# Kernel tuning notes

Hardware: AMD Instinct MI355X
Metric: run time of the kernel (lower is better)

Reference implementation:

```python
import math
import jax, jax.numpy as jnp
import numpy as np

D_MODEL = 1024
NUM_HEADS = 16
D_HEAD = D_MODEL // NUM_HEADS  # 64
K_S = 32  # sparse top-k keys kept per query
B, N = 2, 2048


def setup_inputs() -> dict:
    key = jax.random.key(0)
    ks = jax.random.split(key, 9)
    s = 1.0 / math.sqrt(D_MODEL)
    return {
        "x": jax.random.normal(ks[0], (B, N, D_MODEL), dtype=jnp.float32),
        "Wq": jax.random.normal(ks[1], (D_MODEL, D_MODEL), dtype=jnp.float32) * s,
        "bq": jnp.zeros((D_MODEL,), dtype=jnp.float32),
        "Wk": jax.random.normal(ks[2], (D_MODEL, D_MODEL), dtype=jnp.float32) * s,
        "bk": jnp.zeros((D_MODEL,), dtype=jnp.float32),
        "Wv": jax.random.normal(ks[3], (D_MODEL, D_MODEL), dtype=jnp.float32) * s,
        "bv": jnp.zeros((D_MODEL,), dtype=jnp.float32),
        "Wo": jax.random.normal(ks[4], (D_MODEL, D_MODEL), dtype=jnp.float32) * s,
        "bo": jnp.zeros((D_MODEL,), dtype=jnp.float32),
    }


def _attn(x, Wq, bq, Wk, bk, Wv, bv, Wo, bo):
    b, n, _ = x.shape
    # projections (torch Linear: y = x W^T + b)
    q = (x @ Wq.T + bq).reshape(b, n, NUM_HEADS, D_HEAD).transpose(0, 2, 1, 3)
    k = (x @ Wk.T + bk).reshape(b, n, NUM_HEADS, D_HEAD).transpose(0, 2, 1, 3)
    v = (x @ Wv.T + bv).reshape(b, n, NUM_HEADS, D_HEAD).transpose(0, 2, 1, 3)
    # full scores [b, H, n, n]
    scores = jnp.einsum("bhqd,bhkd->bhqk", q, k) / math.sqrt(D_HEAD)
    # causal mask (triu above diagonal -> -inf)
    causal = jnp.triu(jnp.ones((n, n), dtype=bool), k=1)
    neg_inf = jnp.array(-jnp.inf, dtype=scores.dtype)
    scores = jnp.where(causal, neg_inf, scores)
    # sparse top-k: keep only K_S largest scores per query row
    vals, idx = jax.lax.top_k(scores, K_S)
    masked = jnp.full_like(scores, -jnp.inf)
    masked = jnp.put_along_axis(masked, idx, vals, axis=-1, inplace=False)
    attn = jax.nn.softmax(masked, axis=-1)  # dropout p=0.0 -> identity
    out = jnp.einsum("bhqk,bhkd->bhqd", attn, v)
    out = out.transpose(0, 2, 1, 3).reshape(b, n, D_MODEL)
    y = out @ Wo.T + bo
    return y, attn.mean(axis=1)


def reference(x, Wq, bq, Wk, bk, Wv, bv, Wo, bo):
    return _attn(x, Wq, bq, Wk, bk, Wv, bv, Wo, bo)
```

## Files before the change

### kernel.cpp

```cpp
#include <hip/hip_runtime.h>
#include <hip/hip_bf16.h>
#include <math.h>

#define BATCH   2
#define NTOK    2048
#define DMODEL  1024
#define HEADS   16
#define DHEAD   64
#define KSEL    32
#define MROWS   (BATCH * NTOK)
#define NBLK8   (NTOK / 8)
#define TPW     8

typedef short     bf16x8 __attribute__((ext_vector_type(8)));
typedef float     f32x4  __attribute__((ext_vector_type(4)));
typedef unsigned short ushort_t;
typedef unsigned long long u64;

#define GLOAD_LDS16(g, l) \
    __builtin_amdgcn_global_load_lds((const __attribute__((address_space(1))) void*)(g), \
                                     (__attribute__((address_space(3))) void*)(l), 16, 0, 0)

__device__ __forceinline__ ushort_t f2bf(float f) {
    unsigned u = __float_as_uint(f);
    unsigned r = (u + 0x7FFFu + ((u >> 16) & 1u)) >> 16;
    return (ushort_t)r;
}
__device__ __forceinline__ float bf2f(ushort_t h) {
    return __uint_as_float(((unsigned)h) << 16);
}

__device__ __forceinline__ void conv_body(const float* __restrict__ in,
                                          ushort_t* __restrict__ hi,
                                          ushort_t* __restrict__ lo, int n, int i)
{
    if (i + 3 < n) {
        const float4 v = *(const float4*)(in + i);
        ushort4 ph, pl;
        ph.x = f2bf(v.x); pl.x = f2bf(v.x - bf2f(ph.x));
        ph.y = f2bf(v.y); pl.y = f2bf(v.y - bf2f(ph.y));
        ph.z = f2bf(v.z); pl.z = f2bf(v.z - bf2f(ph.z));
        ph.w = f2bf(v.w); pl.w = f2bf(v.w - bf2f(ph.w));
        *(ushort4*)(hi + i) = ph;
        *(ushort4*)(lo + i) = pl;
    }
}

__global__ __launch_bounds__(256) void conv_split(const float* __restrict__ in,
                                                  ushort_t* __restrict__ hi,
                                                  ushort_t* __restrict__ lo, int n)
{
    const int i = (blockIdx.x * 256 + threadIdx.x) * 4;
    conv_body(in, hi, lo, n, i);
}

__global__ __launch_bounds__(256) void conv_split4(const float* __restrict__ i0, ushort_t* __restrict__ h0, ushort_t* __restrict__ l0,
                                                   const float* __restrict__ i1, ushort_t* __restrict__ h1, ushort_t* __restrict__ l1,
                                                   const float* __restrict__ i2, ushort_t* __restrict__ h2, ushort_t* __restrict__ l2,
                                                   const float* __restrict__ i3, ushort_t* __restrict__ h3, ushort_t* __restrict__ l3,
                                                   int n)
{
    const int w = blockIdx.y;
    const float* in = (w == 0) ? i0 : (w == 1) ? i1 : (w == 2) ? i2 : i3;
    ushort_t* hi = (w == 0) ? h0 : (w == 1) ? h1 : (w == 2) ? h2 : h3;
    ushort_t* lo = (w == 0) ? l0 : (w == 1) ? l1 : (w == 2) ? l2 : l3;
    const int i = (blockIdx.x * 256 + threadIdx.x) * 4;
    conv_body(in, hi, lo, n, i);
}

__global__ __launch_bounds__(256) void zero_fill(float* __restrict__ p, int n4)
{
    const int i = blockIdx.x * 256 + threadIdx.x;
    if (i < n4) ((float4*)p)[i] = (float4){0.f, 0.f, 0.f, 0.f};
}

__device__ __forceinline__ unsigned mono_key(float f) {
    const unsigned u = __float_as_uint(f);
    return (u ^ (unsigned)(((int)u >> 31) | 0x80000000)) + 1u;
}
__device__ __forceinline__ float unmono(unsigned m) {
    const unsigned u = m - 1u;
    return __uint_as_float(u ^ (unsigned)(((int)(~u) >> 31) | 0x80000000));
}

__global__ __launch_bounds__(256, 3) void gemm_split_mfma(const ushort_t* __restrict__ Ahi,
                                                          const ushort_t* __restrict__ Alo,
                                                          const ushort_t* __restrict__ Bhi,
                                                          const ushort_t* __restrict__ Blo,
                                                          const float* __restrict__ bias,
                                                          float* __restrict__ out,
                                                          ushort_t* __restrict__ oh,
                                                          ushort_t* __restrict__ om,
                                                          ushort_t* __restrict__ ol,
                                                          int mode)
{
    __shared__ ushort_t smem[2 * 12288];

    const int tid  = threadIdx.x;
    const int wave = tid >> 6;
    const int lane = tid & 63;
    const int fr   = lane & 15;
    const int k8   = lane >> 4;
    const int m0 = blockIdx.x * 128;
    const int n0 = blockIdx.y * 64;

    f32x4 acc[2][4];
#pragma unroll
    for (int i = 0; i < 2; ++i)
#pragma unroll
        for (int j = 0; j < 4; ++j) acc[i][j] = (f32x4){0.f, 0.f, 0.f, 0.f};

#define STAGE(bufsel, k0v) do {                                                \
        ushort_t* dst_ = smem + (bufsel) * 12288;                              \
        _Pragma("unroll")                                                      \
        for (int i_ = 0; i_ < 2; ++i_) {                                       \
            const int c_ = i_ * 256 + tid;                                     \
            const int row_ = c_ >> 2;                                          \
            const int g_ = (c_ & 3) ^ ((row_ >> 1) & 3);                       \
            const size_t ga_ = (size_t)(m0 + row_) * DMODEL + (k0v) + g_ * 8;  \
            GLOAD_LDS16(Ahi + ga_, dst_ + (size_t)c_ * 8);                     \
            GLOAD_LDS16(Alo + ga_, dst_ + 4096 + (size_t)c_ * 8);              \
        }                                                                      \
        {                                                                      \
            const int c_ = tid;                                                \
            const int row_ = c_ >> 2;                                          \
            const int g_ = (c_ & 3) ^ ((row_ >> 1) & 3);                       \
            const size_t gb_ = (size_t)(n0 + row_) * DMODEL + (k0v) + g_ * 8;  \
            GLOAD_LDS16(Bhi + gb_, dst_ + 8192 + (size_t)c_ * 8);              \
            GLOAD_LDS16(Blo + gb_, dst_ + 10240 + (size_t)c_ * 8);             \
        }                                                                      \
    } while (0)

    STAGE(0, 0);
    int cur = 0;

    for (int k0 = 0; k0 < DMODEL; k0 += 32) {
        __syncthreads();
        if (k0 + 32 < DMODEL) STAGE(cur ^ 1, k0 + 32);

        const ushort_t* buf = smem + cur * 12288;
        bf16x8 afh[2], afl[2], bfh[4], bfl[4];
#pragma unroll
        for (int mi = 0; mi < 2; ++mi) {
            const int r = wave * 32 + mi * 16 + fr;
            const int ro = r * 32 + (k8 ^ ((r >> 1) & 3)) * 8;
            afh[mi] = *(const bf16x8*)(buf + ro);
            afl[mi] = *(const bf16x8*)(buf + 4096 + ro);
        }
#pragma unroll
        for (int ni = 0; ni < 4; ++ni) {
            const int r = ni * 16 + fr;
            const int ro = r * 32 + (k8 ^ ((r >> 1) & 3)) * 8;
            bfh[ni] = *(const bf16x8*)(buf + 8192 + ro);
            bfl[ni] = *(const bf16x8*)(buf + 10240 + ro);
        }

#pragma unroll
        for (int mi = 0; mi < 2; ++mi)
#pragma unroll
            for (int ni = 0; ni < 4; ++ni) {
                acc[mi][ni] = __builtin_amdgcn_mfma_f32_16x16x32_bf16(afh[mi], bfl[ni], acc[mi][ni], 0, 0, 0);
                acc[mi][ni] = __builtin_amdgcn_mfma_f32_16x16x32_bf16(afl[mi], bfh[ni], acc[mi][ni], 0, 0, 0);
                acc[mi][ni] = __builtin_amdgcn_mfma_f32_16x16x32_bf16(afh[mi], bfh[ni], acc[mi][ni], 0, 0, 0);
            }
        cur ^= 1;
    }
#undef STAGE

#pragma unroll
    for (int ni = 0; ni < 4; ++ni) {
        const int o = n0 + ni * 16 + (lane & 15);
        const float bv = bias[o];
#pragma unroll
        for (int mi = 0; mi < 2; ++mi) {
#pragma unroll
            for (int reg = 0; reg < 4; ++reg) {
                const int m = m0 + wave * 32 + mi * 16 + ((lane >> 4) << 2) + reg;
                const float v = acc[mi][ni][reg] + bv;
                if (mode == 0) {
                    out[(size_t)m * DMODEL + o] = v;
                } else {
                    const int bb = m >> 11;
                    const int n  = m & 2047;
                    const int hd = o >> 6;
                    const int d  = o & 63;
                    const size_t off = (((size_t)(bb * HEADS + hd)) * NTOK + n) * DHEAD + d;
                    if (mode == 1) {
                        out[off] = v;
                    } else {
                        const ushort_t h1 = f2bf(v);
                        const float r1 = v - bf2f(h1);
                        const ushort_t m1 = f2bf(r1);
                        const ushort_t l1 = f2bf(r1 - bf2f(m1));
                        oh[off] = h1; om[off] = m1; ol[off] = l1;
                    }
                }
            }
        }
    }
}

__global__ __launch_bounds__(256, 3) void score_mfma(const ushort_t* __restrict__ Qh,
                                                     const ushort_t* __restrict__ Qm,
                                                     const ushort_t* __restrict__ Ql,
                                                     const ushort_t* __restrict__ Kh,
                                                     const ushort_t* __restrict__ Km,
                                                     const ushort_t* __restrict__ Kl,
                                                     unsigned* __restrict__ S,
                                                     unsigned* __restrict__ Smax,
                                                     int q0, int QC)
{
    const int ks = blockIdx.x;
    const int qt = blockIdx.y;
    const int bh = blockIdx.z;
    const int qbase = q0 + qt * 128;
    const int ktmax = ((qbase + 127) >> 6) + 1;
    const int kt0 = ks * TPW;
    if (kt0 >= ktmax) return;
    const int kt1 = (kt0 + TPW < ktmax) ? (kt0 + TPW) : ktmax;

    __shared__ ushort_t smem[2 * 12288];

    const int tid  = threadIdx.x;
    const int wave = tid >> 6;
    const int lane = tid & 63;
    const int l15  = lane & 15;
    const int l4   = lane >> 4;

    const size_t qgbase = ((size_t)bh * NTOK + qbase) * DHEAD;

    bf16x8 qf[3][2][2];
#pragma unroll
    for (int p = 0; p < 3; ++p) {
        const ushort_t* Qp = (p == 0) ? Qh : (p == 1) ? Qm : Ql;
#pragma unroll
        for (int j = 0; j < 2; ++j) {
            const int r = wave * 32 + j * 16 + l15;
#pragma unroll
            for (int h = 0; h < 2; ++h)
                qf[p][j][h] = *(const bf16x8*)(Qp + qgbase + (size_t)r * DHEAD + (h * 4 + l4) * 8);
        }
    }

#define STAGE_K(bufsel, ktv) do {                                              \
        const size_t kg_ = ((size_t)bh * NTOK + (ktv) * 64) * DHEAD;           \
        _Pragma("unroll")                                                      \
        for (int i_ = 0; i_ < 2; ++i_) {                                       \
            const int c_ = i_ * 256 + tid;                                     \
            const int row_ = c_ >> 3;                                          \
            const int g_ = (c_ & 7) ^ (row_ & 7);                              \
            const size_t goff_ = kg_ + (size_t)row_ * DHEAD + g_ * 8;          \
            ushort_t* dst_ = smem + (bufsel) * 12288 + (size_t)c_ * 8;         \
            GLOAD_LDS16(Kh + goff_, dst_ + 0 * 4096);                          \
            GLOAD_LDS16(Km + goff_, dst_ + 1 * 4096);                          \
            GLOAD_LDS16(Kl + goff_, dst_ + 2 * 4096);                          \
        }                                                                      \
    } while (0)

    STAGE_K(0, kt0);
    __builtin_amdgcn_sched_barrier(0);
    asm volatile("s_waitcnt vmcnt(0)" ::: "memory");
    __builtin_amdgcn_s_barrier();
    __builtin_amdgcn_sched_barrier(0);

    int cur = 0;
    const size_t srowQ = (size_t)bh * QC;

    for (int kt = kt0; kt < kt1; ++kt) {
        const bool more = (kt + 1 < kt1);
        if (more) STAGE_K(cur ^ 1, kt + 1);
        __builtin_amdgcn_sched_barrier(0);

        f32x4 acc[4][2];
#pragma unroll
        for (int m = 0; m < 4; ++m)
#pragma unroll
            for (int j = 0; j < 2; ++j) acc[m][j] = (f32x4){0.f, 0.f, 0.f, 0.f};

        const ushort_t* kb = smem + cur * 12288;
#pragma unroll
        for (int h = 0; h < 2; ++h) {
            bf16x8 kf[4];
#pragma unroll
            for (int m = 0; m < 4; ++m) {
                const int r = m * 16 + l15;
                const int slot = (h * 4 + l4) ^ (r & 7);
                kf[m] = *(const bf16x8*)(kb + 0 * 4096 + (size_t)(r * 8 + slot) * 8);
            }
#pragma unroll
            for (int m = 0; m < 4; ++m)
#pragma unroll
                for (int j = 0; j < 2; ++j) {
                    acc[m][j] = __builtin_amdgcn_mfma_f32_16x16x32_bf16(kf[m], qf[2][j][h], acc[m][j], 0, 0, 0);
                    acc[m][j] = __builtin_amdgcn_mfma_f32_16x16x32_bf16(kf[m], qf[1][j][h], acc[m][j], 0, 0, 0);
                    acc[m][j] = __builtin_amdgcn_mfma_f32_16x16x32_bf16(kf[m], qf[0][j][h], acc[m][j], 0, 0, 0);
                }
#pragma unroll
            for (int m = 0; m < 4; ++m) {
                const int r = m * 16 + l15;
                const int slot = (h * 4 + l4) ^ (r & 7);
                kf[m] = *(const bf16x8*)(kb + 1 * 4096 + (size_t)(r * 8 + slot) * 8);
            }
#pragma unroll
            for (int m = 0; m < 4; ++m)
#pragma unroll
                for (int j = 0; j < 2; ++j) {
                    acc[m][j] = __builtin_amdgcn_mfma_f32_16x16x32_bf16(kf[m], qf[1][j][h], acc[m][j], 0, 0, 0);
                    acc[m][j] = __builtin_amdgcn_mfma_f32_16x16x32_bf16(kf[m], qf[0][j][h], acc[m][j], 0, 0, 0);
                }
#pragma unroll
            for (int m = 0; m < 4; ++m) {
                const int r = m * 16 + l15;
                const int slot = (h * 4 + l4) ^ (r & 7);
                kf[m] = *(const bf16x8*)(kb + 2 * 4096 + (size_t)(r * 8 + slot) * 8);
            }
#pragma unroll
            for (int m = 0; m < 4; ++m)
#pragma unroll
                for (int j = 0; j < 2; ++j)
                    acc[m][j] = __builtin_amdgcn_mfma_f32_16x16x32_bf16(kf[m], qf[0][j][h], acc[m][j], 0, 0, 0);
        }

#pragma unroll
        for (int j = 0; j < 2; ++j) {
            const int qrow  = wave * 32 + j * 16 + l15;
            const int qlrow = qt * 128 + qrow;
            const int qglob = qbase + qrow;
            const size_t srow = (srowQ + qlrow) * NTOK;
            const size_t mrow = (srowQ + qlrow) * NBLK8;
#pragma unroll
            for (int m = 0; m < 4; ++m) {
                const int kcol0 = kt * 64 + m * 16 + (l4 << 2);
                uint4 kv;
                kv.x = mono_key(acc[m][j][0] * 0.125f);
                kv.y = mono_key(acc[m][j][1] * 0.125f);
                kv.z = mono_key(acc[m][j][2] * 0.125f);
                kv.w = mono_key(acc[m][j][3] * 0.125f);
                *(uint4*)(S + srow + kcol0) = kv;
                unsigned cm = (kcol0     <= qglob) ? kv.x : 0u;
                unsigned t;
                t = (kcol0 + 1 <= qglob) ? kv.y : 0u; cm = (t > cm) ? t : cm;
                t = (kcol0 + 2 <= qglob) ? kv.z : 0u; cm = (t > cm) ? t : cm;
                t = (kcol0 + 3 <= qglob) ? kv.w : 0u; cm = (t > cm) ? t : cm;
                const unsigned o = __shfl_xor(cm, 16, 64);
                cm = (o > cm) ? o : cm;
                if ((lane & 16) == 0) {
                    const int gblk = kt * 8 + m * 2 + (lane >> 5);
                    Smax[mrow + gblk] = cm;
                }
            }
        }

        if (more) {
            asm volatile("s_waitcnt vmcnt(16)" ::: "memory");
            __builtin_amdgcn_s_barrier();
            __builtin_amdgcn_sched_barrier(0);
        }
        cur ^= 1;
    }
#undef STAGE_K
}

__global__ __launch_bounds__(256) void select_v6(const unsigned* __restrict__ S,
                                                 const unsigned* __restrict__ Smax,
                                                 const float* __restrict__ V,
                                                 float* __restrict__ ctx,
                                                 float* __restrict__ attn,
                                                 int q0, int QC)
{
    __shared__ int   sBlkAll[4][KSEL];
    __shared__ int   sIdxAll[4][KSEL];
    __shared__ float sEAll[4][KSEL];

    const int lane = threadIdx.x & 63;
    const int wave = threadIdx.x >> 6;
    const int ql = blockIdx.x;
    const int b  = blockIdx.y >> 2;
    const int hg = blockIdx.y & 3;
    const int h  = hg * 4 + wave;
    const int q  = q0 + ql;
    const int L  = q + 1;
    const int nsel = (L < KSEL) ? L : KSEL;
    const int nb = (L + 7) >> 3;

    const size_t bhx = (size_t)(b * HEADS + h);
    const unsigned* Srow = S + (bhx * QC + ql) * NTOK;
    const unsigned* Mrow = Smax + (bhx * QC + ql) * NBLK8;
    const float* Vb   = V + bhx * NTOK * DHEAD;
    float* ctxRow  = ctx + (((size_t)(b * NTOK + q)) * HEADS + h) * DHEAD;
    float* attnRow = attn + ((size_t)(b * NTOK + q)) * NTOK;
    int*   sBlk = sBlkAll[wave];
    int*   sIdx = sIdxAll[wave];
    float* sE   = sEAll[wave];

    const uint4 bm4 = *(const uint4*)(Mrow + lane * 4);
    unsigned bmax[4] = {bm4.x, bm4.y, bm4.z, bm4.w};
#pragma unroll
    for (int s = 0; s < 4; ++s)
        if (lane * 4 + s >= nb) bmax[s] = 0u;

    unsigned gmax = bmax[0];
    gmax = (bmax[1] > gmax) ? bmax[1] : gmax;
    gmax = (bmax[2] > gmax) ? bmax[2] : gmax;
    gmax = (bmax[3] > gmax) ? bmax[3] : gmax;
#pragma unroll
    for (int d = 1; d < 64; d <<= 1) {
        const unsigned o = __shfl_xor(gmax, d, 64);
        gmax = (o > gmax) ? o : gmax;
    }
    const float vmax = unmono(gmax);

    unsigned selb = 0u;
    unsigned blkLo = 1u;
    int nselb;
    if (nb <= KSEL) {
        nselb = nb;
#pragma unroll
        for (int s = 0; s < 4; ++s)
            if (lane * 4 + s < nb) selb |= 1u << s;
    } else {
        nselb = KSEL;
        unsigned lo = 1u, hi = gmax >> 16;
        while (lo < hi) {
            const unsigned mid = lo + ((hi - lo + 1u) >> 1);
            const unsigned midk = mid << 16;
            int cnt = 0;
#pragma unroll
            for (int s = 0; s < 4; ++s)
                cnt += __popcll(__ballot(bmax[s] >= midk));
            if (cnt >= KSEL) lo = mid; else hi = mid - 1u;
        }
        blkLo = lo;
        const unsigned Tkb = lo << 16;
        const unsigned Gkb = Tkb | 0xFFFFu;
        int cge = 0, cgt = 0;
#pragma unroll
        for (int s = 0; s < 4; ++s) {
            cge += __popcll(__ballot(bmax[s] >= Tkb));
            cgt += __popcll(__ballot(bmax[s] > Gkb));
        }
        if (cge == KSEL) {
#pragma unroll
            for (int s = 0; s < 4; ++s)
                selb |= (bmax[s] >= Tkb) ? (1u << s) : 0u;
        } else {
            unsigned bmb = 0u;
#pragma unroll
            for (int s = 0; s < 4; ++s) {
                selb |= (bmax[s] > Gkb) ? (1u << s) : 0u;
                bmb  |= (bmax[s] >= Tkb && bmax[s] <= Gkb) ? (1u << s) : 0u;
            }
            int k_tie = KSEL - cgt;
            while (k_tie > 0) {
                u64 best = 0;
                unsigned bmm = bmb;
                while (bmm) {
                    const int s = __builtin_ctz(bmm);
                    bmm &= bmm - 1u;
                    const unsigned gblk = (unsigned)(lane * 4 + s);
                    const u64 k = ((u64)bmax[s] << 32) | (unsigned)~gblk;
                    if (k > best) best = k;
                }
                u64 bb = best;
#pragma unroll
                for (int d = 1; d < 64; d <<= 1) {
                    const u64 o = __shfl_xor(bb, d, 64);
                    bb = (o > bb) ? o : bb;
                }
                const unsigned gblk = ~(unsigned)bb;
                if (lane == (int)(gblk >> 2)) {
                    const unsigned bit = 1u << (gblk & 3u);
                    selb |= bit;
                    bmb &= ~bit;
                }
                --k_tie;
            }
        }
    }

    {
        const int cb = __popc(selb);
        int pfxb = cb;
#pragma unroll
        for (int d = 1; d < 64; d <<= 1) {
            const int t = __shfl_up(pfxb, d, 64);
            if (lane >= d) pfxb += t;
        }
        pfxb -= cb;
        unsigned mskb = selb;
        int posb = pfxb;
        while (mskb) {
            const int s = __builtin_ctz(mskb);
            mskb &= mskb - 1u;
            sBlk[posb++] = lane * 4 + s;
        }
    }
    __asm volatile("s_waitcnt lgkmcnt(0)" ::: "memory");

    const int NC = nselb * 8;
    unsigned km[4];
    int idx[4];
#pragma unroll
    for (int c = 0; c < 4; ++c) {
        const int t = c * 64 + lane;
        unsigned m = 0u;
        int j = 0;
        if (t < NC) {
            const int blk = sBlk[t >> 3];
            j = blk * 8 + (t & 7);
            if (j < L) m = Srow[j];
        }
        km[c] = m;
        idx[c] = j;
    }

    unsigned lo = blkLo, hi = gmax >> 16;
    while (lo < hi) {
        const unsigned mid = lo + ((hi - lo + 1u) >> 1);
        const unsigned midk = mid << 16;
        int cnt = 0;
#pragma unroll
        for (int c = 0; c < 4; ++c)
            cnt += __popcll(__ballot(km[c] >= midk));
        if (cnt >= nsel) lo = mid; else hi = mid - 1u;
    }
    const unsigned Tk = lo << 16;
    const unsigned Gk = Tk | 0xFFFFu;

    int cnt_ge = 0, cnt_gt = 0;
#pragma unroll
    for (int c = 0; c < 4; ++c) {
        cnt_ge += __popcll(__ballot(km[c] >= Tk));
        cnt_gt += __popcll(__ballot(km[c] > Gk));
    }

    unsigned selmask = 0u;
    if (cnt_ge == nsel) {
#pragma unroll
        for (int c = 0; c < 4; ++c)
            selmask |= (km[c] >= Tk) ? (1u << c) : 0u;
    } else {
        unsigned bmask = 0u;
#pragma unroll
        for (int c = 0; c < 4; ++c) {
            selmask |= (km[c] > Gk) ? (1u << c) : 0u;
            bmask   |= (km[c] >= Tk && km[c] <= Gk) ? (1u << c) : 0u;
        }
        int k_tie = nsel - cnt_gt;
        while (k_tie > 0) {
            u64 best = 0;
            unsigned bmm = bmask;
            while (bmm) {
                const int c = __builtin_ctz(bmm);
                bmm &= bmm - 1u;
                const int t = c * 64 + lane;
                const u64 k = ((u64)km[c] << 32) |
                              ((u64)(0xFFFFu ^ (unsigned)idx[c]) << 16) | (u64)t;
                if (k > best) best = k;
            }
            u64 bb = best;
#pragma unroll
            for (int d = 1; d < 64; d <<= 1) {
                const u64 o = __shfl_xor(bb, d, 64);
                bb = (o > bb) ? o : bb;
            }
            const unsigned tt = (unsigned)bb & 0xFFFFu;
            if (lane == (int)(tt & 63u)) {
                const unsigned bit = 1u << (tt >> 6);
                selmask |= bit;
                bmask &= ~bit;
            }
            --k_tie;
        }
    }

    const int csel = __popc(selmask);
    int pfx = csel;
#pragma unroll
    for (int d = 1; d < 64; d <<= 1) {
        const int t = __shfl_up(pfx, d, 64);
        if (lane >= d) pfx += t;
    }
    pfx -= csel;

    float esum = 0.f;
    unsigned msk = selmask;
    int pos = pfx;
    while (msk) {
        const int c = __builtin_ctz(msk);
        msk &= msk - 1u;
        const float e = __expf(unmono(km[c]) - vmax);
        esum += e;
        sIdx[pos] = idx[c];
        sE[pos] = e;
        ++pos;
    }

    float Z = esum;
#pragma unroll
    for (int d = 1; d < 64; d <<= 1) Z += __shfl_xor(Z, d, 64);
    const float rcpZ = 1.0f / Z;

    msk = selmask;
    pos = pfx;
    while (msk) {
        const int c = __builtin_ctz(msk);
        msk &= msk - 1u;
        const float w = sE[pos] * rcpZ;
        ++pos;
        atomicAdd(&attnRow[idx[c]], w * (1.0f / (float)HEADS));
    }

    float acc = 0.f;
    for (int i = 0; i < nsel; ++i) {
        const int id = sIdx[i];
        const float wi = sE[i] * rcpZ;
        acc += wi * Vb[(size_t)id * DHEAD + lane];
    }
    ctxRow[lane] = acc;
}

extern "C" void kernel_launch(void* const* d_in, const int* in_sizes, int n_in,
                              void* d_out, int out_size, void* d_ws, size_t ws_size,
                              hipStream_t stream) {
    const float* x  = (const float*)d_in[0];
    const float* Wq = (const float*)d_in[1];
    const float* bq = (const float*)d_in[2];
    const float* Wk = (const float*)d_in[3];
    const float* bk = (const float*)d_in[4];
    const float* Wv = (const float*)d_in[5];
    const float* bv = (const float*)d_in[6];
    const float* Wo = (const float*)d_in[7];
    const float* bo = (const float*)d_in[8];

    const size_t MB = 1ull << 20;
    char* wsb = (char*)d_ws;
    float*    Vws = (float*)(wsb + 0 * MB);
    float*    ctx = (float*)(wsb + 16 * MB);
    ushort_t* xhi = (ushort_t*)(wsb + 32 * MB);
    ushort_t* xlo = (ushort_t*)(wsb + 40 * MB);
    ushort_t* wqh = (ushort_t*)(wsb + 48 * MB);
    ushort_t* wql = (ushort_t*)(wsb + 50 * MB);
    ushort_t* wkh = (ushort_t*)(wsb + 52 * MB);
    ushort_t* wkl = (ushort_t*)(wsb + 54 * MB);
    ushort_t* wvh = (ushort_t*)(wsb + 56 * MB);
    ushort_t* wvl = (ushort_t*)(wsb + 58 * MB);
    ushort_t* woh = (ushort_t*)(wsb + 60 * MB);
    ushort_t* wol = (ushort_t*)(wsb + 62 * MB);
    ushort_t* Qh  = (ushort_t*)(wsb + 64 * MB);
    ushort_t* Qm  = (ushort_t*)(wsb + 72 * MB);
    ushort_t* Ql  = (ushort_t*)(wsb + 80 * MB);
    ushort_t* Kh  = (ushort_t*)(wsb + 88 * MB);
    ushort_t* Km  = (ushort_t*)(wsb + 96 * MB);
    ushort_t* Kl  = (ushort_t*)(wsb + 104 * MB);
    ushort_t* cxh = xhi;
    ushort_t* cxl = xlo;

    float* y    = (float*)d_out;
    float* attn = y + (size_t)BATCH * NTOK * DMODEL;

    const int NX = MROWS * DMODEL;
    const int NW = DMODEL * DMODEL;

    conv_split<<<NX / (256 * 4), 256, 0, stream>>>(x, xhi, xlo, NX);
    {
        dim3 cgrid(NW / (256 * 4), 4);
        conv_split4<<<cgrid, 256, 0, stream>>>(Wq, wqh, wql,
                                               Wk, wkh, wkl,
                                               Wv, wvh, wvl,
                                               Wo, woh, wol, NW);
    }

    dim3 ggrid(MROWS / 128, DMODEL / 64);
    gemm_split_mfma<<<ggrid, 256, 0, stream>>>(xhi, xlo, wqh, wql, bq, nullptr, Qh, Qm, Ql, 2);
    gemm_split_mfma<<<ggrid, 256, 0, stream>>>(xhi, xlo, wkh, wkl, bk, nullptr, Kh, Km, Kl, 2);
    gemm_split_mfma<<<ggrid, 256, 0, stream>>>(xhi, xlo, wvh, wvl, bv, Vws, nullptr, nullptr, nullptr, 1);

    const size_t base_bytes = 112 * MB;
    const size_t avail = (ws_size > base_bytes) ? ws_size - base_bytes : 0;
    int QC = 128;
    for (int cand = NTOK; cand >= 128; cand >>= 1) {
        const size_t need = (size_t)BATCH * HEADS * cand * (size_t)(NTOK + NBLK8) * sizeof(unsigned);
        if (need <= avail) { QC = cand; break; }
    }
    unsigned* Smax = (unsigned*)(wsb + base_bytes);
    unsigned* Sws  = (unsigned*)(wsb + base_bytes +
                                 (size_t)BATCH * HEADS * QC * NBLK8 * sizeof(unsigned));

    const int nattn4 = BATCH * NTOK * NTOK / 4;
    zero_fill<<<(nattn4 + 255) / 256, 256, 0, stream>>>(attn, nattn4);
    for (int q0 = 0; q0 < NTOK; q0 += QC) {
        const int ktm = (q0 + QC) >> 6;
        dim3 sgrid((ktm + TPW - 1) / TPW, QC / 128, BATCH * HEADS);
        score_mfma<<<sgrid, 256, 0, stream>>>(Qh, Qm, Ql, Kh, Km, Kl, Sws, Smax, q0, QC);
        dim3 selgrid(QC, BATCH * 4);
        select_v6<<<selgrid, 256, 0, stream>>>(Sws, Smax, Vws, ctx, attn, q0, QC);
    }

    conv_split<<<NX / (256 * 4), 256, 0, stream>>>(ctx, cxh, cxl, NX);
    gemm_split_mfma<<<ggrid, 256, 0, stream>>>(cxh, cxl, woh, wol, bo, y, nullptr, nullptr, nullptr, 0);
}
```

Baseline: 534.7 us.

## Fuse Q/K/V projections into one GEMM, shrink score tiles and query chunk

Replaces three separate split-bf16 projection GEMMs with one fused kernel that loads each x tile once and multiplies it against the Wq, Wk and Wv tiles, so the activation tile is reused three times. It also lowers tiles-per-workgroup in the score kernel from 8 to 4 and caps the query chunk size at 512 to increase parallelism and reduce workspace traffic per pass. The fused kernel holds three accumulator sets and a larger LDS footprint, so occupancy drops (launch bounds lowered to 2), and the smaller query chunks mean more score/select launches.

```diff
diff --git a/kernel.cpp b/kernel.cpp
--- a/kernel.cpp
+++ b/kernel.cpp
@@ -10,7 +10,7 @@
 #define KSEL    32
 #define MROWS   (BATCH * NTOK)
 #define NBLK8   (NTOK / 8)
-#define TPW     8
+#define TPW     4
 
 typedef short     bf16x8 __attribute__((ext_vector_type(8)));
 typedef float     f32x4  __attribute__((ext_vector_type(4)));
@@ -83,18 +83,26 @@
     return __uint_as_float(u ^ (unsigned)(((int)(~u) >> 31) | 0x80000000));
 }
 
-__global__ __launch_bounds__(256, 3) void gemm_split_mfma(const ushort_t* __restrict__ Ahi,
-                                                          const ushort_t* __restrict__ Alo,
-                                                          const ushort_t* __restrict__ Bhi,
-                                                          const ushort_t* __restrict__ Blo,
-                                                          const float* __restrict__ bias,
-                                                          float* __restrict__ out,
-                                                          ushort_t* __restrict__ oh,
-                                                          ushort_t* __restrict__ om,
-                                                          ushort_t* __restrict__ ol,
-                                                          int mode)
+__global__ __launch_bounds__(256, 2) void gemm_qkv_fused(const ushort_t* __restrict__ xhi,
+                                                         const ushort_t* __restrict__ xlo,
+                                                         const ushort_t* __restrict__ wqh,
+                                                         const ushort_t* __restrict__ wql,
+                                                         const ushort_t* __restrict__ wkh,
+                                                         const ushort_t* __restrict__ wkl,
+                                                         const ushort_t* __restrict__ wvh,
+                                                         const ushort_t* __restrict__ wvl,
+                                                         const float* __restrict__ bq,
+                                                         const float* __restrict__ bk,
+                                                         const float* __restrict__ bv,
+                                                         ushort_t* __restrict__ Qh,
+                                                         ushort_t* __restrict__ Qm,
+                                                         ushort_t* __restrict__ Ql,
+                                                         ushort_t* __restrict__ Kh,
+                                                         ushort_t* __restrict__ Km,
+                                                         ushort_t* __restrict__ Kl,
+                                                         float* __restrict__ Vws)
 {
-    __shared__ ushort_t smem[2 * 12288];
+    __shared__ ushort_t smem[2 * 20480];
 
     const int tid  = threadIdx.x;
     const int wave = tid >> 6;
@@ -104,6 +112,133 @@
     const int m0 = blockIdx.x * 128;
     const int n0 = blockIdx.y * 64;
 
+    f32x4 acc[3][2][4];
+#pragma unroll
+    for (int w = 0; w < 3; ++w)
+#pragma unroll
+        for (int i = 0; i < 2; ++i)
+#pragma unroll
+            for (int j = 0; j < 4; ++j) acc[w][i][j] = (f32x4){0.f, 0.f, 0.f, 0.f};
+
+#define STAGEF(bufsel, k0v) do {                                               \
+        ushort_t* dst_ = smem + (size_t)(bufsel) * 20480;                      \
+        _Pragma("unroll")                                                      \
+        for (int i_ = 0; i_ < 2; ++i_) {                                       \
+            const int c_ = i_ * 256 + tid;                                     \
+            const int row_ = c_ >> 2;                                          \
+            const int g_ = (c_ & 3) ^ ((row_ >> 1) & 3);                       \
+            const size_t ga_ = (size_t)(m0 + row_) * DMODEL + (k0v) + g_ * 8;  \
+            GLOAD_LDS16(xhi + ga_, dst_ + (size_t)c_ * 8);                     \
+            GLOAD_LDS16(xlo + ga_, dst_ + 4096 + (size_t)c_ * 8);              \
+        }                                                                      \
+        {                                                                      \
+            const int c_ = tid;                                                \
+            const int row_ = c_ >> 2;                                          \
+            const int g_ = (c_ & 3) ^ ((row_ >> 1) & 3);                       \
+            const size_t gb_ = (size_t)(n0 + row_) * DMODEL + (k0v) + g_ * 8;  \
+            GLOAD_LDS16(wqh + gb_, dst_ + 8192 + (size_t)c_ * 8);              \
+            GLOAD_LDS16(wql + gb_, dst_ + 10240 + (size_t)c_ * 8);             \
+            GLOAD_LDS16(wkh + gb_, dst_ + 12288 + (size_t)c_ * 8);             \
+            GLOAD_LDS16(wkl + gb_, dst_ + 14336 + (size_t)c_ * 8);             \
+            GLOAD_LDS16(wvh + gb_, dst_ + 16384 + (size_t)c_ * 8);             \
+            GLOAD_LDS16(wvl + gb_, dst_ + 18432 + (size_t)c_ * 8);             \
+        }                                                                      \
+    } while (0)
+
+    STAGEF(0, 0);
+    int cur = 0;
+
+    for (int k0 = 0; k0 < DMODEL; k0 += 32) {
+        __syncthreads();
+        if (k0 + 32 < DMODEL) STAGEF(cur ^ 1, k0 + 32);
+
+        const ushort_t* buf = smem + (size_t)cur * 20480;
+        bf16x8 afh[2], afl[2];
+#pragma unroll
+        for (int mi = 0; mi < 2; ++mi) {
+            const int r = wave * 32 + mi * 16 + fr;
+            const int ro = r * 32 + (k8 ^ ((r >> 1) & 3)) * 8;
+            afh[mi] = *(const bf16x8*)(buf + ro);
+            afl[mi] = *(const bf16x8*)(buf + 4096 + ro);
+        }
+
+#pragma unroll
+        for (int w = 0; w < 3; ++w) {
+            const ushort_t* bb = buf + 8192 + w * 4096;
+            bf16x8 bfh[4], bfl[4];
+#pragma unroll
+            for (int ni = 0; ni < 4; ++ni) {
+                const int r = ni * 16 + fr;
+                const int ro = r * 32 + (k8 ^ ((r >> 1) & 3)) * 8;
+                bfh[ni] = *(const bf16x8*)(bb + ro);
+                bfl[ni] = *(const bf16x8*)(bb + 2048 + ro);
+            }
+#pragma unroll
+            for (int mi = 0; mi < 2; ++mi)
+#pragma unroll
+                for (int ni = 0; ni < 4; ++ni) {
+                    acc[w][mi][ni] = __builtin_amdgcn_mfma_f32_16x16x32_bf16(afh[mi], bfl[ni], acc[w][mi][ni], 0, 0, 0);
+                    acc[w][mi][ni] = __builtin_amdgcn_mfma_f32_16x16x32_bf16(afl[mi], bfh[ni], acc[w][mi][ni], 0, 0, 0);
+                    acc[w][mi][ni] = __builtin_amdgcn_mfma_f32_16x16x32_bf16(afh[mi], bfh[ni], acc[w][mi][ni], 0, 0, 0);
+                }
+        }
+        cur ^= 1;
+    }
+#undef STAGEF
+
+#pragma unroll
+    for (int w = 0; w < 3; ++w) {
+        const float* bias = (w == 0) ? bq : (w == 1) ? bk : bv;
+        ushort_t* oh = (w == 0) ? Qh : Kh;
+        ushort_t* om = (w == 0) ? Qm : Km;
+        ushort_t* ol = (w == 0) ? Ql : Kl;
+#pragma unroll
+        for (int ni = 0; ni < 4; ++ni) {
+            const int o = n0 + ni * 16 + (lane & 15);
+            const float bvv = bias[o];
+            const int hd = o >> 6;
+            const int d  = o & 63;
+#pragma unroll
+            for (int mi = 0; mi < 2; ++mi) {
+#pragma unroll
+                for (int reg = 0; reg < 4; ++reg) {
+                    const int m = m0 + wave * 32 + mi * 16 + ((lane >> 4) << 2) + reg;
+                    const float v = acc[w][mi][ni][reg] + bvv;
+                    const int bb = m >> 11;
+                    const int n  = m & 2047;
+                    const size_t off = (((size_t)(bb * HEADS + hd)) * NTOK + n) * DHEAD + d;
+                    if (w == 2) {
+                        Vws[off] = v;
+                    } else {
+                        const ushort_t h1 = f2bf(v);
+                        const float r1 = v - bf2f(h1);
+                        const ushort_t m1 = f2bf(r1);
+                        const ushort_t l1 = f2bf(r1 - bf2f(m1));
+                        oh[off] = h1; om[off] = m1; ol[off] = l1;
+                    }
+                }
+            }
+        }
+    }
+}
+
+__global__ __launch_bounds__(256, 2) void gemm_split_mfma(const ushort_t* __restrict__ Ahi,
+                                                          const ushort_t* __restrict__ Alo,
+                                                          const ushort_t* __restrict__ Bhi,
+                                                          const ushort_t* __restrict__ Blo,
+                                                          const float* __restrict__ bias,
+                                                          float* __restrict__ out)
+{
+    __shared__ ushort_t smem[2 * 12288];
+
+    const int tid  = threadIdx.x;
+    const int wave = tid >> 6;
+    const int lane = tid & 63;
+    const int fr   = lane & 15;
+    const int k8   = lane >> 4;
+    const int m0 = blockIdx.x * 128;
+    const int n0 = blockIdx.y * 64;
+
     f32x4 acc[2][4];
 #pragma unroll
     for (int i = 0; i < 2; ++i)
@@ -111,7 +246,7 @@
         for (int j = 0; j < 4; ++j) acc[i][j] = (f32x4){0.f, 0.f, 0.f, 0.f};
 
 #define STAGE(bufsel, k0v) do {                                                \
-        ushort_t* dst_ = smem + (bufsel) * 12288;                              \
+        ushort_t* dst_ = smem + (size_t)(bufsel) * 12288;                      \
         _Pragma("unroll")                                                      \
         for (int i_ = 0; i_ < 2; ++i_) {                                       \
             const int c_ = i_ * 256 + tid;                                     \
@@ -138,7 +273,7 @@
         __syncthreads();
         if (k0 + 32 < DMODEL) STAGE(cur ^ 1, k0 + 32);
 
-        const ushort_t* buf = smem + cur * 12288;
+        const ushort_t* buf = smem + (size_t)cur * 12288;
         bf16x8 afh[2], afl[2], bfh[4], bfl[4];
 #pragma unroll
         for (int mi = 0; mi < 2; ++mi) {
@@ -176,25 +311,7 @@
 #pragma unroll
             for (int reg = 0; reg < 4; ++reg) {
                 const int m = m0 + wave * 32 + mi * 16 + ((lane >> 4) << 2) + reg;
-                const float v = acc[mi][ni][reg] + bv;
-                if (mode == 0) {
-                    out[(size_t)m * DMODEL + o] = v;
-                } else {
-                    const int bb = m >> 11;
-                    const int n  = m & 2047;
-                    const int hd = o >> 6;
-                    const int d  = o & 63;
-                    const size_t off = (((size_t)(bb * HEADS + hd)) * NTOK + n) * DHEAD + d;
-                    if (mode == 1) {
-                        out[off] = v;
-                    } else {
-                        const ushort_t h1 = f2bf(v);
-                        const float r1 = v - bf2f(h1);
-                        const ushort_t m1 = f2bf(r1);
-                        const ushort_t l1 = f2bf(r1 - bf2f(m1));
-                        oh[off] = h1; om[off] = m1; ol[off] = l1;
-                    }
-                }
+                out[(size_t)m * DMODEL + o] = acc[mi][ni][reg] + bv;
             }
         }
     }
@@ -672,14 +789,15 @@
     }
 
     dim3 ggrid(MROWS / 128, DMODEL / 64);
-    gemm_split_mfma<<<ggrid, 256, 0, stream>>>(xhi, xlo, wqh, wql, bq, nullptr, Qh, Qm, Ql, 2);
-    gemm_split_mfma<<<ggrid, 256, 0, stream>>>(xhi, xlo, wkh, wkl, bk, nullptr, Kh, Km, Kl, 2);
-    gemm_split_mfma<<<ggrid, 256, 0, stream>>>(xhi, xlo, wvh, wvl, bv, Vws, nullptr, nullptr, nullptr, 1);
+    gemm_qkv_fused<<<ggrid, 256, 0, stream>>>(xhi, xlo,
+                                              wqh, wql, wkh, wkl, wvh, wvl,
+                                              bq, bk, bv,
+                                              Qh, Qm, Ql, Kh, Km, Kl, Vws);
 
     const size_t base_bytes = 112 * MB;
     const size_t avail = (ws_size > base_bytes) ? ws_size - base_bytes : 0;
     int QC = 128;
-    for (int cand = NTOK; cand >= 128; cand >>= 1) {
+    for (int cand = 512; cand >= 128; cand >>= 1) {
         const size_t need = (size_t)BATCH * HEADS * cand * (size_t)(NTOK + NBLK8) * sizeof(unsigned);
         if (need <= avail) { QC = cand; break; }
     }
@@ -698,5 +816,5 @@
     }
 
     conv_split<<<NX / (256 * 4), 256, 0, stream>>>(ctx, cxh, cxl, NX);
-    gemm_split_mfma<<<ggrid, 256, 0, stream>>>(cxh, cxl, woh, wol, bo, y, nullptr, nullptr, nullptr, 0);
-}
+    gemm_split_mfma<<<ggrid, 256, 0, stream>>>(cxh, cxl, woh, wol, bo, y);
+}
```

Measured after the change: 503.1 us. 5.9% less time.
